# Kernel optimization log

Hardware: AMD Instinct MI355X
Metric: run time of the kernel (lower is better)

## Reference

```python
import jax, jax.numpy as jnp
import numpy as np

WS = 8          # window_size
NH = 8          # num_heads
DIM = 512
INNER = 512
CDIM = 128
CINNER = 128
SHIFTED = True
EPS = 1e-6
N = WS * WS     # tokens per window
SCALE = 1.0 / np.sqrt(INNER // NH + CINNER // NH)  # SDPA scale over fused (feat+coord) head dim


def _rmsnorm(x, g):
    return x * jax.lax.rsqrt(jnp.mean(x * x, axis=-1, keepdims=True) + EPS) * g


def _rel_indices():
    idx = np.array([[x, y] for x in range(WS) for y in range(WS)])
    ri = idx[None, :, :] - idx[:, None, :] + WS - 1
    return ri[..., 0], ri[..., 1]


def _shift_mask(Wh, Ww):
    s = WS
    k = s * (s // 2)
    row = np.zeros((N, N), np.float32)
    row[-k:, :-k] = -np.inf
    row[:-k, -k:] = -np.inf
    col = row.reshape(s, s, s, s).transpose(1, 0, 3, 2).reshape(N, N)
    m = np.zeros((Wh, Ww, N, N), np.float32)
    m[:, -1] += row
    m[-1, :] += col
    return jnp.asarray(m)


def setup_inputs() -> dict:
    key = jax.random.key(0)
    ks = jax.random.split(key, 16)
    B, h, w = 4, 128, 128

    def lin(k, fan_in, fan_out):
        return jax.random.normal(k, (fan_in, fan_out), jnp.float32) * (fan_in ** -0.5)

    return {
        "features": jax.random.normal(ks[0], (B, h, w, DIM), jnp.float32),
        "coords": jax.random.normal(ks[1], (B, h, w, CDIM), jnp.float32),
        "w_fqk": lin(ks[2], DIM, 2 * INNER),
        "b_fqk": jnp.zeros((2 * INNER,), jnp.float32),
        "g_fqk": jnp.ones((2 * INNER,), jnp.float32),
        "w_cqk": lin(ks[3], CDIM, 2 * CINNER),
        "b_cqk": jnp.zeros((2 * CINNER,), jnp.float32),
        "g_cqk": jnp.ones((2 * CINNER,), jnp.float32),
        "w_v": lin(ks[4], DIM, INNER),
        "b_v": jnp.zeros((INNER,), jnp.float32),
        "w_out": lin(ks[5], INNER, DIM),
        "b_out": jnp.zeros((DIM,), jnp.float32),
        "pos_emb": jax.random.normal(ks[6], (2 * WS - 1, 2 * WS - 1), jnp.float32),
    }


def reference(features, coords, w_fqk, b_fqk, g_fqk, w_cqk, b_cqk, g_cqk,
              w_v, b_v, w_out, b_out, pos_emb):
    B, h, w, _ = features.shape
    pad_h = (WS - h % WS) % WS
    pad_w = (WS - w % WS) % WS
    H_pad, W_pad = h + pad_h, w + pad_w
    Wh, Ww = H_pad // WS, W_pad // WS

    fqk = _rmsnorm(features @ w_fqk + b_fqk, g_fqk)
    f_q, f_k = jnp.split(fqk, 2, axis=-1)
    cqk = _rmsnorm(coords @ w_cqk + b_cqk, g_cqk)
    c_q, c_k = jnp.split(cqk, 2, axis=-1)
    f_v = features @ w_v + b_v

    def win(t):
        t = jnp.pad(t, ((0, 0), (0, pad_h), (0, pad_w), (0, 0)))
        if SHIFTED:
            t = jnp.roll(t, (-(WS // 2), -(WS // 2)), axis=(1, 2))
        D = t.shape[-1]
        t = t.reshape(B, Wh, WS, Ww, WS, D).transpose(0, 1, 3, 2, 4, 5)
        return t.reshape(B, Wh, Ww, N, D)

    def heads(t):
        D = t.shape[-1]
        return t.reshape(B, Wh, Ww, N, NH, D // NH)

    fq, fk, fv = heads(win(f_q)), heads(win(f_k)), heads(win(f_v))
    cq, ck = heads(win(c_q)), heads(win(c_k))

    # fused feature + coordinate QK scores, per head per window
    scores = (jnp.einsum('bxyqhd,bxykhd->bxyhqk', fq, fk)
              + jnp.einsum('bxyqhd,bxykhd->bxyhqk', cq, ck)) * SCALE

    ri0, ri1 = _rel_indices()
    pos_bias = pos_emb[ri0, ri1]  # (N, N)
    bias = pos_bias[None, None, None, None]
    if SHIFTED:
        bias = bias + _shift_mask(Wh, Ww)[None, :, :, None]
    scores = scores + bias

    attn = jax.nn.softmax(scores, axis=-1)
    out = jnp.einsum('bxyhqk,bxykhd->bxyqhd', attn, fv)
    out = out.reshape(B, Wh, Ww, N, INNER)

    # un-window
    out = out.reshape(B, Wh, Ww, WS, WS, INNER).transpose(0, 1, 3, 2, 4, 5)
    out = out.reshape(B, H_pad, W_pad, INNER)
    if SHIFTED:
        out = jnp.roll(out, (WS // 2, WS // 2), axis=(1, 2))
    out = out[:, :h, :w, :]
    return out @ w_out + b_out
```

## Files before the change

kernel.cpp:

```cpp
#include <hip/hip_runtime.h>
#include <hip/hip_bf16.h>
#include <type_traits>

using bf16 = __hip_bfloat16;
typedef __bf16 bf16x8 __attribute__((ext_vector_type(8)));
typedef float f32x4 __attribute__((ext_vector_type(4)));

static constexpr int TOKENS = 4 * 128 * 128;
#define SCALE_F 0.11180339887498949f
#define EPS_F 1e-6f

__device__ __forceinline__ float u2f(unsigned short u) {
  union { unsigned int i; float f; } c; c.i = (unsigned int)u << 16; return c.f;
}
__device__ __forceinline__ unsigned short f2u(float f) {
  bf16 h = __float2bfloat16(f); return *reinterpret_cast<unsigned short*>(&h);
}
__device__ __forceinline__ float b2f(bf16 v) { return __bfloat162float(v); }
__device__ __forceinline__ int4 cvt8(const float* p) {
  float4 a = ((const float4*)p)[0], b = ((const float4*)p)[1];
  union { int4 i4; unsigned short s[8]; } u;
  u.s[0] = f2u(a.x); u.s[1] = f2u(a.y); u.s[2] = f2u(a.z); u.s[3] = f2u(a.w);
  u.s[4] = f2u(b.x); u.s[5] = f2u(b.y); u.s[6] = f2u(b.z); u.s[7] = f2u(b.w);
  return u.i4;
}
__device__ __forceinline__ void gload16(const bf16* g, bf16* l) {
  __builtin_amdgcn_global_load_lds(
      (const __attribute__((address_space(1))) unsigned int*)g,
      (__attribute__((address_space(3))) unsigned int*)l, 16, 0, 0);
}

__global__ void convert_k(const float* __restrict__ in, bf16* __restrict__ out,
                          long n) {
  long i = ((long)blockIdx.x * 256 + threadIdx.x) * 8;
  long stride = (long)gridDim.x * 256 * 8;
  for (; i < n; i += stride) *(int4*)(out + i) = cvt8(in + i);
}

__global__ void transpose_k(const float* __restrict__ in, bf16* __restrict__ out,
                            int K, int N) {
  int i = blockIdx.x * 256 + threadIdx.x;
  if (i >= K * N) return;
  int k = i / N, n = i - k * N;
  out[(size_t)n * K + k] = __float2bfloat16(in[i]);
}

__global__ void biascat_k(const float* __restrict__ a, const float* __restrict__ b,
                          float* __restrict__ o) {
  int i = blockIdx.x * 256 + threadIdx.x;
  if (i < 1536) o[i] = i < 1024 ? a[i] : b[i - 1024];
}

__global__ void gains_k(const float* __restrict__ g_fqk,
                        const float* __restrict__ g_cqk,
                        float* __restrict__ gf, float* __restrict__ gc) {
  int i = blockIdx.x * 256 + threadIdx.x;
  if (i < 512) gf[i] = g_fqk[i] * g_fqk[512 + i];
  else if (i < 640) { int d = i - 512; gc[d] = g_cqk[d] * g_cqk[128 + d]; }
}

template <typename TC, int SSNX, int GS>
__global__ __launch_bounds__(512, 2) void gemm256p_k(
    const bf16* __restrict__ A, const bf16* __restrict__ Wt,
    const float* __restrict__ bias, TC* __restrict__ C,
    float* __restrict__ ssq, const float* __restrict__ gsc,
    int M, int N, int K) {
  extern __shared__ __align__(16) bf16 smem[];
  bf16* sW = smem;
  bf16* sX = smem + 32768;
  const int t = threadIdx.x, lane = t & 63, wave = t >> 6;
  const int wm = wave >> 2, wn = wave & 3;
  const int l15 = lane & 15, kg = lane >> 4;
  const int nwg = gridDim.x * gridDim.y;
  int id = blockIdx.y * gridDim.x + blockIdx.x;
  id = (id & 7) * (nwg >> 3) + (id >> 3);
  const int bx = id % gridDim.x, by = id / gridDim.x;
  const int bm = by * 256, bn = bx * 256;
  f32x4 acc[8][4] = {};

  const int lr = t >> 3, ch = t & 7;
  const int ssw = ((ch ^ (lr & 7)) * 8);
  const int rsw = (l15 & 7) * 8;

  auto stW = [&](int buf, int fh, int k0) {
#pragma unroll
    for (int g = 0; g < 2; ++g)
      gload16(Wt + (size_t)(bn + g * 128 + fh * 64 + lr) * K + k0 + ssw,
              sW + buf * 16384 + (fh * 128 + g * 64) * 64 + t * 8);
  };
  auto stX = [&](int buf, int th, int k0) {
#pragma unroll
    for (int g = 0; g < 2; ++g)
      gload16(A + (size_t)(bm + (g * 2 + (lr >> 5)) * 64 + th * 32 + (lr & 31)) * K + k0 + ssw,
              sX + buf * 16384 + (th * 128 + g * 64) * 64 + t * 8);
  };
  auto rdW = [&](int buf, int fh, int i, int ks) {
    int row = fh * 128 + wm * 64 + i * 16 + l15;
    return *(const bf16x8*)(sW + buf * 16384 + row * 64 + ((ks * 32 + kg * 8) ^ rsw));
  };
  auto rdX = [&](int buf, int th, int j, int ks) {
    int row = th * 128 + wn * 32 + j * 16 + l15;
    return *(const bf16x8*)(sX + buf * 16384 + row * 64 + ((ks * 32 + kg * 8) ^ rsw));
  };

  const int NT = K >> 6;
  stW(0, 0, 0); stX(0, 0, 0); stX(0, 1, 0); stW(0, 1, 0);

  bf16x8 wfr[4][2], xf0[2][2], xf1[2][2];
  for (int u = 0; u < NT; ++u) {
    const int buf = u & 1, nbuf = buf ^ 1, k1 = (u + 1) << 6;
    const bool pf = (u + 1 < NT);
    asm volatile("s_waitcnt vmcnt(4)" ::: "memory");
    __builtin_amdgcn_s_barrier();
    __builtin_amdgcn_sched_barrier(0);
#pragma unroll
    for (int i = 0; i < 4; ++i)
#pragma unroll
      for (int ks = 0; ks < 2; ++ks) wfr[i][ks] = rdW(buf, 0, i, ks);
#pragma unroll
    for (int j = 0; j < 2; ++j)
#pragma unroll
      for (int ks = 0; ks < 2; ++ks) xf0[j][ks] = rdX(buf, 0, j, ks);
    if (pf) { stW(nbuf, 0, k1); stX(nbuf, 0, k1); }
    asm volatile("s_waitcnt lgkmcnt(0)" ::: "memory");
    __builtin_amdgcn_sched_barrier(0);
    __builtin_amdgcn_s_setprio(1);
#pragma unroll
    for (int i = 0; i < 4; ++i)
#pragma unroll
      for (int j = 0; j < 2; ++j)
#pragma unroll
        for (int ks = 0; ks < 2; ++ks)
          acc[i][j] = __builtin_amdgcn_mfma_f32_16x16x32_bf16(wfr[i][ks], xf0[j][ks], acc[i][j], 0, 0, 0);
    __builtin_amdgcn_s_setprio(0);
    if (pf) asm volatile("s_waitcnt vmcnt(6)" ::: "memory");
    else    asm volatile("s_waitcnt vmcnt(2)" ::: "memory");
    __builtin_amdgcn_s_barrier();
    __builtin_amdgcn_sched_barrier(0);
#pragma unroll
    for (int j = 0; j < 2; ++j)
#pragma unroll
      for (int ks = 0; ks < 2; ++ks) xf1[j][ks] = rdX(buf, 1, j, ks);
    if (pf) stX(nbuf, 1, k1);
    asm volatile("s_waitcnt lgkmcnt(0)" ::: "memory");
    __builtin_amdgcn_sched_barrier(0);
    __builtin_amdgcn_s_setprio(1);
#pragma unroll
    for (int i = 0; i < 4; ++i)
#pragma unroll
      for (int j = 0; j < 2; ++j)
#pragma unroll
        for (int ks = 0; ks < 2; ++ks)
          acc[i][2 + j] = __builtin_amdgcn_mfma_f32_16x16x32_bf16(wfr[i][ks], xf1[j][ks], acc[i][2 + j], 0, 0, 0);
    __builtin_amdgcn_s_setprio(0);
    if (pf) asm volatile("s_waitcnt vmcnt(6)" ::: "memory");
    else    asm volatile("s_waitcnt vmcnt(0)" ::: "memory");
    __builtin_amdgcn_s_barrier();
    __builtin_amdgcn_sched_barrier(0);
#pragma unroll
    for (int i = 0; i < 4; ++i)
#pragma unroll
      for (int ks = 0; ks < 2; ++ks) wfr[i][ks] = rdW(buf, 1, i, ks);
    if (pf) stW(nbuf, 1, k1);
    asm volatile("s_waitcnt lgkmcnt(0)" ::: "memory");
    __builtin_amdgcn_sched_barrier(0);
    __builtin_amdgcn_s_setprio(1);
#pragma unroll
    for (int i = 0; i < 4; ++i)
#pragma unroll
      for (int j = 0; j < 2; ++j)
#pragma unroll
        for (int ks = 0; ks < 2; ++ks)
          acc[4 + i][j] = __builtin_amdgcn_mfma_f32_16x16x32_bf16(wfr[i][ks], xf0[j][ks], acc[4 + i][j], 0, 0, 0);
    __builtin_amdgcn_s_setprio(0);
    __builtin_amdgcn_s_barrier();
    __builtin_amdgcn_sched_barrier(0);
    __builtin_amdgcn_s_setprio(1);
#pragma unroll
    for (int i = 0; i < 4; ++i)
#pragma unroll
      for (int j = 0; j < 2; ++j)
#pragma unroll
        for (int ks = 0; ks < 2; ++ks)
          acc[4 + i][2 + j] = __builtin_amdgcn_mfma_f32_16x16x32_bf16(wfr[i][ks], xf1[j][ks], acc[4 + i][2 + j], 0, 0, 0);
    __builtin_amdgcn_s_setprio(0);
  }

  float bvi[8][4];
#pragma unroll
  for (int fi = 0; fi < 8; ++fi) {
    float4 b4 = *(const float4*)(bias + bn + wm * 128 + (fi >> 2) * 64 + (fi & 3) * 16 + kg * 4);
    bvi[fi][0] = b4.x; bvi[fi][1] = b4.y; bvi[fi][2] = b4.z; bvi[fi][3] = b4.w;
  }
#pragma unroll
  for (int tj = 0; tj < 4; ++tj) {
    const int token = bm + wn * 64 + (tj >> 1) * 32 + (tj & 1) * 16 + l15;
    float ssum = 0.f;
#pragma unroll
    for (int fi = 0; fi < 8; ++fi) {
      const int fo = wm * 128 + (fi >> 2) * 64 + (fi & 3) * 16 + kg * 4;
      float v0 = acc[fi][tj][0] + bvi[fi][0];
      float v1 = acc[fi][tj][1] + bvi[fi][1];
      float v2 = acc[fi][tj][2] + bvi[fi][2];
      float v3 = acc[fi][tj][3] + bvi[fi][3];
      if constexpr (SSNX > 0)
        ssum += v0 * v0 + v1 * v1 + v2 * v2 + v3 * v3;
      if constexpr (GS) {
        const int col = bn + fo;
        if (col >= 512 && col < 1024) {
          float4 g4 = *(const float4*)(gsc + (col - 512));
          v0 *= g4.x; v1 *= g4.y; v2 *= g4.z; v3 *= g4.w;
        }
      }
      const size_t off = (size_t)token * N + bn + fo;
      if constexpr (std::is_same<TC, float>::value) {
        *(float4*)(C + off) = float4{v0, v1, v2, v3};
      } else {
        ushort4 pk{f2u(v0), f2u(v1), f2u(v2), f2u(v3)};
        *(ushort4*)(C + off) = pk;
      }
    }
    if constexpr (SSNX > 0) {
      ssum += __shfl_xor(ssum, 16);
      ssum += __shfl_xor(ssum, 32);
      if (bx < SSNX && kg == 0)
        ssq[(size_t)token * (SSNX * 2) + bx * 2 + wm] = ssum;
    }
  }
}

template <typename TC, int SSNX, int GS>
__global__ __launch_bounds__(256) void gemm128_k(
    const bf16* __restrict__ A, const bf16* __restrict__ Wt,
    const float* __restrict__ bias, TC* __restrict__ C,
    float* __restrict__ ssq, const float* __restrict__ gsc,
    int M, int N, int K) {
  __shared__ __align__(16) bf16 sA[2][4096];
  __shared__ __align__(16) bf16 sB[2][4096];
  const int t = threadIdx.x, lane = t & 63, wave = t >> 6;
  const int wr = wave >> 1, wc = wave & 1;
  const int nwg = gridDim.x * gridDim.y;
  int id = blockIdx.y * gridDim.x + blockIdx.x;
  if ((nwg & 7) == 0) id = (id & 7) * (nwg >> 3) + (id >> 3);
  const int bx = id % gridDim.x, by = id / gridDim.x;
  const int bm = by * 128, bn = bx * 128;
  const int l15 = lane & 15, kg = lane >> 4;
  f32x4 acc[4][4] = {};

  const int srow = t >> 2;
  const int ske = ((t & 3) ^ ((srow >> 1) & 3)) * 8;
  const bf16* pA0 = A + (size_t)(bm + srow) * K + ske;
  const bf16* pA1 = A + (size_t)(bm + 64 + srow) * K + ske;
  const bf16* pB0 = Wt + (size_t)(bn + srow) * K + ske;
  const bf16* pB1 = Wt + (size_t)(bn + 64 + srow) * K + ske;
  const int wo = wave * 512;

  gload16(pA0, &sA[0][wo]);
  gload16(pA1, &sA[0][2048 + wo]);
  gload16(pB0, &sB[0][wo]);
  gload16(pB1, &sB[0][2048 + wo]);
  __syncthreads();

  const int nt = K >> 5;
  int cur = 0;
  for (int tt = 0; tt < nt; ++tt) {
    if (tt + 1 < nt) {
      pA0 += 32; pA1 += 32; pB0 += 32; pB1 += 32;
      gload16(pA0, &sA[cur ^ 1][wo]);
      gload16(pA1, &sA[cur ^ 1][2048 + wo]);
      gload16(pB0, &sB[cur ^ 1][wo]);
      gload16(pB1, &sB[cur ^ 1][2048 + wo]);
    }
    bf16x8 wf[4], xf[4];
#pragma unroll
    for (int i = 0; i < 4; ++i) {
      int frow = wc * 64 + i * 16 + l15;
      int xrow = wr * 64 + i * 16 + l15;
      wf[i] = *(const bf16x8*)(&sB[cur][frow * 32 + ((kg ^ ((frow >> 1) & 3)) * 8)]);
      xf[i] = *(const bf16x8*)(&sA[cur][xrow * 32 + ((kg ^ ((xrow >> 1) & 3)) * 8)]);
    }
#pragma unroll
    for (int i = 0; i < 4; ++i)
#pragma unroll
      for (int j = 0; j < 4; ++j)
        acc[i][j] = __builtin_amdgcn_mfma_f32_16x16x32_bf16(wf[i], xf[j], acc[i][j], 0, 0, 0);
    __syncthreads();
    cur ^= 1;
  }

  float bvi[4][4];
#pragma unroll
  for (int i = 0; i < 4; ++i) {
    float4 b4 = *(const float4*)(bias + bn + wc * 64 + i * 16 + kg * 4);
    bvi[i][0] = b4.x; bvi[i][1] = b4.y; bvi[i][2] = b4.z; bvi[i][3] = b4.w;
  }
#pragma unroll
  for (int j = 0; j < 4; ++j) {
    const int token = bm + wr * 64 + j * 16 + l15;
    float ssum = 0.f;
#pragma unroll
    for (int i = 0; i < 4; ++i) {
      const int fo = wc * 64 + i * 16 + kg * 4;
      float v0 = acc[i][j][0] + bvi[i][0];
      float v1 = acc[i][j][1] + bvi[i][1];
      float v2 = acc[i][j][2] + bvi[i][2];
      float v3 = acc[i][j][3] + bvi[i][3];
      if constexpr (SSNX > 0)
        ssum += v0 * v0 + v1 * v1 + v2 * v2 + v3 * v3;
      if constexpr (GS) {
        const int col = bn + fo;
        if (col >= 128 && col < 256) {
          float4 g4 = *(const float4*)(gsc + (col - 128));
          v0 *= g4.x; v1 *= g4.y; v2 *= g4.z; v3 *= g4.w;
        }
      }
      const size_t off = (size_t)token * N + bn + fo;
      if constexpr (std::is_same<TC, float>::value) {
        *(float4*)(C + off) = float4{v0, v1, v2, v3};
      } else {
        ushort4 pk{f2u(v0), f2u(v1), f2u(v2), f2u(v3)};
        *(ushort4*)(C + off) = pk;
      }
    }
    if constexpr (SSNX > 0) {
      ssum += __shfl_xor(ssum, 16);
      ssum += __shfl_xor(ssum, 32);
      if (bx < SSNX && kg == 0)
        ssq[(size_t)token * (SSNX * 2) + bx * 2 + wc] = ssum;
    }
  }
}

__global__ void finalize_rs_k(const float* __restrict__ pf,
                              const float* __restrict__ pc,
                              float* __restrict__ rsf, float* __restrict__ rsc) {
  int i = blockIdx.x * 256 + threadIdx.x;
  if (i >= TOKENS) return;
  float s = 0.f;
#pragma unroll
  for (int j = 0; j < 8; ++j) s += pf[(size_t)i * 8 + j];
  rsf[i] = rsqrtf(s * (1.f / 1024.f) + EPS_F);
  float c = 0.f;
#pragma unroll
  for (int j = 0; j < 4; ++j) c += pc[(size_t)i * 4 + j];
  rsc[i] = rsqrtf(c * (1.f / 256.f) + EPS_F);
}

__global__ __launch_bounds__(256) void attn_mfma_k(
    const bf16* __restrict__ qkv, const bf16* __restrict__ cqk,
    const float* __restrict__ pos, const float* __restrict__ rs_f,
    const float* __restrict__ rs_c, bf16* __restrict__ aout) {
  __shared__ __align__(16) bf16 sQ[64][104], sK[64][104];
  __shared__ __align__(16) bf16 sVt[64][72];
  __shared__ __align__(16) bf16 sP[64][72];
  __shared__ float sPos[15][15];
  __shared__ float sRsF[64], sRsC[64];
  const int t = threadIdx.x, lane = t & 63, wave = t >> 6;
  const int head = blockIdx.x & 7;
  const int wid = blockIdx.x >> 3;
  const int wx = wid & 15, wy = (wid >> 4) & 15, b = wid >> 8;

  for (int i = t; i < 225; i += 256) sPos[i / 15][i % 15] = pos[i];
  if (t < 64) {
    const int y = ((wy << 3) + (t >> 3) + 4) & 127;
    const int x = ((wx << 3) + (t & 7) + 4) & 127;
    const size_t tok = ((size_t)b << 14) | (y << 7) | x;
    sRsF[t] = rs_f[tok];
    sRsC[t] = rs_c[tok];
  }
  {
    const int n = t >> 2, p = t & 3;
    const int y = ((wy << 3) + (n >> 3) + 4) & 127;
    const int x = ((wx << 3) + (n & 7) + 4) & 127;
    const size_t tok = ((size_t)b << 14) | (y << 7) | x;
    const bf16* row = qkv + tok * 1536;
    const int4* qp = (const int4*)(row + head * 64 + p * 16);
    ((int4*)&sQ[n][p * 16])[0] = qp[0];
    ((int4*)&sQ[n][p * 16])[1] = qp[1];
    const int4* kp = (const int4*)(row + 512 + head * 64 + p * 16);
    ((int4*)&sK[n][p * 16])[0] = kp[0];
    ((int4*)&sK[n][p * 16])[1] = kp[1];
    const bf16* vp = row + 1024 + head * 64 + p * 16;
#pragma unroll
    for (int i = 0; i < 16; ++i) sVt[p * 16 + i][n] = vp[i];
    const bf16* crow = cqk + tok * 256;
    if (p == 0) {
      const int4* cp = (const int4*)(crow + head * 16);
      ((int4*)&sQ[n][64])[0] = cp[0];
      ((int4*)&sQ[n][64])[1] = cp[1];
    } else if (p == 1) {
      const int4* cp = (const int4*)(crow + 128 + head * 16);
      ((int4*)&sK[n][64])[0] = cp[0];
      ((int4*)&sK[n][64])[1] = cp[1];
    } else if (p == 2) {
      ((int4*)&sQ[n][80])[0] = int4{0, 0, 0, 0};
      ((int4*)&sQ[n][80])[1] = int4{0, 0, 0, 0};
    } else {
      ((int4*)&sK[n][80])[0] = int4{0, 0, 0, 0};
      ((int4*)&sK[n][80])[1] = int4{0, 0, 0, 0};
    }
  }
  __syncthreads();

  const int l15 = lane & 15, kg = lane >> 4;
  bf16x8 qa[3];
#pragma unroll
  for (int ko = 0; ko < 3; ++ko)
    qa[ko] = *(const bf16x8*)&sQ[wave * 16 + l15][ko * 32 + kg * 8];
  f32x4 saccf[4] = {}, saccc[4] = {};
#pragma unroll
  for (int j = 0; j < 4; ++j) {
#pragma unroll
    for (int ko = 0; ko < 2; ++ko) {
      bf16x8 kb = *(const bf16x8*)&sK[j * 16 + l15][ko * 32 + kg * 8];
      saccf[j] = __builtin_amdgcn_mfma_f32_16x16x32_bf16(qa[ko], kb, saccf[j], 0, 0, 0);
    }
    bf16x8 kb2 = *(const bf16x8*)&sK[j * 16 + l15][64 + kg * 8];
    saccc[j] = __builtin_amdgcn_mfma_f32_16x16x32_bf16(qa[2], kb2, saccc[j], 0, 0, 0);
  }

  const bool lastx = (wx == 15), lasty = (wy == 15);
  float rqf[4], rqc[4];
#pragma unroll
  for (int r = 0; r < 4; ++r) {
    rqf[r] = sRsF[wave * 16 + kg * 4 + r];
    rqc[r] = sRsC[wave * 16 + kg * 4 + r];
  }
  float sv[4][4], mx[4], sum[4], inv[4];
#pragma unroll
  for (int r = 0; r < 4; ++r) mx[r] = -1e30f;
#pragma unroll
  for (int j = 0; j < 4; ++j) {
    int kcol = j * 16 + l15, kh = kcol >> 3, kw = kcol & 7;
    float rkf = sRsF[kcol], rkc = sRsC[kcol];
#pragma unroll
    for (int r = 0; r < 4; ++r) {
      int q = wave * 16 + kg * 4 + r, qh = q >> 3, qw = q & 7;
      bool msk = (lastx && ((qh >= 4) != (kh >= 4))) ||
                 (lasty && ((qw >= 4) != (kw >= 4)));
      float raw = saccf[j][r] * rqf[r] * rkf + saccc[j][r] * rqc[r] * rkc;
      float val = msk ? -1e30f : raw * SCALE_F + sPos[kh - qh + 7][kw - qw + 7];
      sv[j][r] = val;
      mx[r] = fmaxf(mx[r], val);
    }
  }
#pragma unroll
  for (int m = 1; m < 16; m <<= 1)
#pragma unroll
    for (int r = 0; r < 4; ++r) mx[r] = fmaxf(mx[r], __shfl_xor(mx[r], m));
#pragma unroll
  for (int r = 0; r < 4; ++r) sum[r] = 0.f;
#pragma unroll
  for (int j = 0; j < 4; ++j) {
    int kcol = j * 16 + l15;
#pragma unroll
    for (int r = 0; r < 4; ++r) {
      float e = __expf(sv[j][r] - mx[r]);
      sum[r] += e;
      sP[wave * 16 + kg * 4 + r][kcol] = __float2bfloat16(e);
    }
  }
#pragma unroll
  for (int m = 1; m < 16; m <<= 1)
#pragma unroll
    for (int r = 0; r < 4; ++r) sum[r] += __shfl_xor(sum[r], m);
#pragma unroll
  for (int r = 0; r < 4; ++r) inv[r] = 1.f / sum[r];
  __syncthreads();

  bf16x8 pa[2];
#pragma unroll
  for (int ko = 0; ko < 2; ++ko)
    pa[ko] = *(const bf16x8*)&sP[wave * 16 + l15][ko * 32 + kg * 8];
  f32x4 oacc[4] = {};
#pragma unroll
  for (int jf = 0; jf < 4; ++jf)
#pragma unroll
    for (int ko = 0; ko < 2; ++ko) {
      bf16x8 vb = *(const bf16x8*)&sVt[jf * 16 + l15][ko * 32 + kg * 8];
      oacc[jf] = __builtin_amdgcn_mfma_f32_16x16x32_bf16(pa[ko], vb, oacc[jf], 0, 0, 0);
    }
#pragma unroll
  for (int r = 0; r < 4; ++r) {
    int q = wave * 16 + kg * 4 + r;
    const int y = ((wy << 3) + (q >> 3) + 4) & 127;
    const int x = ((wx << 3) + (q & 7) + 4) & 127;
    const size_t tok = ((size_t)b << 14) | (y << 7) | x;
    bf16* dst = aout + tok * 512 + head * 64;
#pragma unroll
    for (int jf = 0; jf < 4; ++jf)
      dst[jf * 16 + l15] = __float2bfloat16(oacc[jf][r] * inv[r]);
  }
}

extern "C" void kernel_launch(void* const* d_in, const int* in_sizes, int n_in,
                              void* d_out, int out_size, void* d_ws, size_t ws_size,
                              hipStream_t stream) {
  const float* features = (const float*)d_in[0];
  const float* coords   = (const float*)d_in[1];
  const float* w_fqk = (const float*)d_in[2];
  const float* b_fqk = (const float*)d_in[3];
  const float* g_fqk = (const float*)d_in[4];
  const float* w_cqk = (const float*)d_in[5];
  const float* b_cqk = (const float*)d_in[6];
  const float* g_cqk = (const float*)d_in[7];
  const float* w_v   = (const float*)d_in[8];
  const float* b_v   = (const float*)d_in[9];
  const float* w_out = (const float*)d_in[10];
  const float* b_out = (const float*)d_in[11];
  const float* pos_emb = (const float*)d_in[12];
  float* out = (float*)d_out;

  const int M = TOKENS;
  bf16* qkv   = (bf16*)d_ws;
  bf16* cqk   = qkv + (size_t)M * 1536;
  bf16* aout  = cqk + (size_t)M * 256;
  bf16* wcombT = aout + (size_t)M * 512;
  bf16* wcqkT  = wcombT + (size_t)1536 * 512;
  bf16* woutT  = wcqkT + 256 * 128;
  float* bias_comb = (float*)(woutT + 512 * 512);
  float* ssq_f = bias_comb + 1536;
  float* ssq_c = ssq_f + (size_t)M * 8;
  float* rs_f  = ssq_c + (size_t)M * 4;
  float* rs_c  = rs_f + M;
  float* gf    = rs_c + M;
  float* gc    = gf + 512;
  bf16* fb16 = (bf16*)d_out;
  bf16* cb16 = fb16 + (size_t)M * 512;

  convert_k<<<2048, 256, 0, stream>>>(features, fb16, (long)M * 512);
  convert_k<<<1024, 256, 0, stream>>>(coords, cb16, (long)M * 128);
  transpose_k<<<(512 * 1024 + 255) / 256, 256, 0, stream>>>(w_fqk, wcombT, 512, 1024);
  transpose_k<<<(512 * 512 + 255) / 256, 256, 0, stream>>>(w_v, wcombT + (size_t)1024 * 512, 512, 512);
  transpose_k<<<(128 * 256 + 255) / 256, 256, 0, stream>>>(w_cqk, wcqkT, 128, 256);
  transpose_k<<<(512 * 512 + 255) / 256, 256, 0, stream>>>(w_out, woutT, 512, 512);
  biascat_k<<<6, 256, 0, stream>>>(b_fqk, b_v, bias_comb);
  gains_k<<<3, 256, 0, stream>>>(g_fqk, g_cqk, gf, gc);

  gemm256p_k<bf16, 4, 1><<<dim3(6, 256), 512, 131072, stream>>>(fb16, wcombT, bias_comb, qkv, ssq_f, gf, M, 1536, 512);
  gemm128_k<bf16, 2, 1><<<dim3(2, 512), 256, 0, stream>>>(cb16, wcqkT, b_cqk, cqk, ssq_c, gc, M, 256, 128);
  finalize_rs_k<<<TOKENS / 256, 256, 0, stream>>>(ssq_f, ssq_c, rs_f, rs_c);
  attn_mfma_k<<<4 * 16 * 16 * 8, 256, 0, stream>>>(qkv, cqk, pos_emb, rs_f, rs_c, aout);
  gemm256p_k<float, 0, 0><<<dim3(2, 256), 512, 131072, stream>>>(aout, woutT, b_out, out, nullptr, nullptr, M, 512, 512);
}
```

Baseline: 380.7 us.

## Make GEMM persistent across N tiles with a triple-buffered K=32 pipeline

Replaces the 2D-grid 256x256 GEMM with a kernel where each block owns 256 rows and loops over every N tile (6 for the QKV projection, 2 for the output projection). It uses a 3-stage ring of K=32 slices so global loads run two steps ahead and the pipeline does not drain between N tiles. Bias is staged in LDS once per block. This reduces the grid to 256 blocks with a smaller LDS footprint. The intent is to hide the per-tile prologue/epilogue and keep A rows hot. In exchange there is less parallelism (256 blocks, one wave of work per CU) and a serialized epilogue between tiles. The ssq stride changes to 12, but finalize still reads only 8 of the entries.

```diff
diff --git a/kernel.cpp b/kernel.cpp
--- a/kernel.cpp
+++ b/kernel.cpp
@@ -59,172 +59,138 @@
   else if (i < 640) { int d = i - 512; gc[d] = g_cqk[d] * g_cqk[128 + d]; }
 }
 
-template <typename TC, int SSNX, int GS>
-__global__ __launch_bounds__(512, 2) void gemm256p_k(
+template <typename TC, int EPSSQ, int TPB, int GS>
+__global__ __launch_bounds__(512) void gemm256s_k(
     const bf16* __restrict__ A, const bf16* __restrict__ Wt,
     const float* __restrict__ bias, TC* __restrict__ C,
-    float* __restrict__ ssq, const float* __restrict__ gsc,
-    int M, int N, int K) {
+    float* __restrict__ ssq, const float* __restrict__ gsc, int N) {
+  constexpr int K = 512, GT = 16 * TPB;
   extern __shared__ __align__(16) bf16 smem[];
-  bf16* sW = smem;
-  bf16* sX = smem + 32768;
+  bf16* sX = smem;
+  bf16* sW = smem + 24576;
+  float* sB = (float*)(smem + 49152);
   const int t = threadIdx.x, lane = t & 63, wave = t >> 6;
   const int wm = wave >> 2, wn = wave & 3;
   const int l15 = lane & 15, kg = lane >> 4;
-  const int nwg = gridDim.x * gridDim.y;
-  int id = blockIdx.y * gridDim.x + blockIdx.x;
-  id = (id & 7) * (nwg >> 3) + (id >> 3);
-  const int bx = id % gridDim.x, by = id / gridDim.x;
-  const int bm = by * 256, bn = bx * 256;
+  const int bm = blockIdx.x * 256;
+  const int srow = t >> 2;
+  const int ssw = ((t & 3) ^ ((srow >> 1) & 3)) * 8;
+  const int sdst = t * 8;
+
+  auto stX = [&](int buf, int g) {
+    int k0 = (g & 15) << 5;
+    bf16* d = sX + buf * 8192 + sdst;
+    gload16(A + (size_t)(bm + srow) * K + k0 + ssw, d);
+    gload16(A + (size_t)(bm + 128 + srow) * K + k0 + ssw, d + 4096);
+  };
+  auto stW = [&](int buf, int g) {
+    int k0 = (g & 15) << 5;
+    int bn = (g >> 4) << 8;
+    bf16* d = sW + buf * 8192 + sdst;
+    gload16(Wt + (size_t)(bn + srow) * K + k0 + ssw, d);
+    gload16(Wt + (size_t)(bn + 128 + srow) * K + k0 + ssw, d + 4096);
+  };
+  auto rdX = [&](int buf, int j) {
+    int row = wn * 64 + j * 16 + l15;
+    return *(const bf16x8*)(sX + buf * 8192 + row * 32 + ((kg ^ ((row >> 1) & 3)) * 8));
+  };
+  auto rdW = [&](int buf, int half, int i) {
+    int row = wm * 128 + half * 64 + i * 16 + l15;
+    return *(const bf16x8*)(sW + buf * 8192 + row * 32 + ((kg ^ ((row >> 1) & 3)) * 8));
+  };
+
+  const int nb4 = N / 4;
+  float4 bv4 = float4{0.f, 0.f, 0.f, 0.f};
+  if (t < nb4) bv4 = ((const float4*)bias)[t];
+  stX(0, 0); stW(0, 0); stX(1, 1); stW(1, 1);
+  asm volatile("s_waitcnt vmcnt(8)" ::: "memory");
+  if (t < nb4) ((float4*)sB)[t] = bv4;
+
   f32x4 acc[8][4] = {};
-
-  const int lr = t >> 3, ch = t & 7;
-  const int ssw = ((ch ^ (lr & 7)) * 8);
-  const int rsw = (l15 & 7) * 8;
-
-  auto stW = [&](int buf, int fh, int k0) {
-#pragma unroll
-    for (int g = 0; g < 2; ++g)
-      gload16(Wt + (size_t)(bn + g * 128 + fh * 64 + lr) * K + k0 + ssw,
-              sW + buf * 16384 + (fh * 128 + g * 64) * 64 + t * 8);
-  };
-  auto stX = [&](int buf, int th, int k0) {
-#pragma unroll
-    for (int g = 0; g < 2; ++g)
-      gload16(A + (size_t)(bm + (g * 2 + (lr >> 5)) * 64 + th * 32 + (lr & 31)) * K + k0 + ssw,
-              sX + buf * 16384 + (th * 128 + g * 64) * 64 + t * 8);
-  };
-  auto rdW = [&](int buf, int fh, int i, int ks) {
-    int row = fh * 128 + wm * 64 + i * 16 + l15;
-    return *(const bf16x8*)(sW + buf * 16384 + row * 64 + ((ks * 32 + kg * 8) ^ rsw));
-  };
-  auto rdX = [&](int buf, int th, int j, int ks) {
-    int row = th * 128 + wn * 32 + j * 16 + l15;
-    return *(const bf16x8*)(sX + buf * 16384 + row * 64 + ((ks * 32 + kg * 8) ^ rsw));
-  };
-
-  const int NT = K >> 6;
-  stW(0, 0, 0); stX(0, 0, 0); stX(0, 1, 0); stW(0, 1, 0);
-
-  bf16x8 wfr[4][2], xf0[2][2], xf1[2][2];
-  for (int u = 0; u < NT; ++u) {
-    const int buf = u & 1, nbuf = buf ^ 1, k1 = (u + 1) << 6;
-    const bool pf = (u + 1 < NT);
-    asm volatile("s_waitcnt vmcnt(4)" ::: "memory");
+  int buf = 0;
+  for (int g = 0; g < GT; ++g) {
+    if (g == GT - 1 || (g > 0 && (g & 15) == 0)) {
+      asm volatile("s_waitcnt vmcnt(0)" ::: "memory");
+    } else {
+      asm volatile("s_waitcnt vmcnt(4)" ::: "memory");
+    }
     __builtin_amdgcn_s_barrier();
     __builtin_amdgcn_sched_barrier(0);
-#pragma unroll
-    for (int i = 0; i < 4; ++i)
-#pragma unroll
-      for (int ks = 0; ks < 2; ++ks) wfr[i][ks] = rdW(buf, 0, i, ks);
-#pragma unroll
-    for (int j = 0; j < 2; ++j)
-#pragma unroll
-      for (int ks = 0; ks < 2; ++ks) xf0[j][ks] = rdX(buf, 0, j, ks);
-    if (pf) { stW(nbuf, 0, k1); stX(nbuf, 0, k1); }
+    int nb = buf + 2; if (nb >= 3) nb -= 3;
+    bf16x8 xf[4], wf[4];
+#pragma unroll
+    for (int j = 0; j < 4; ++j) xf[j] = rdX(buf, j);
+#pragma unroll
+    for (int i = 0; i < 4; ++i) wf[i] = rdW(buf, 0, i);
+    if (g + 2 < GT) stX(nb, g + 2);
     asm volatile("s_waitcnt lgkmcnt(0)" ::: "memory");
     __builtin_amdgcn_sched_barrier(0);
     __builtin_amdgcn_s_setprio(1);
 #pragma unroll
     for (int i = 0; i < 4; ++i)
 #pragma unroll
-      for (int j = 0; j < 2; ++j)
-#pragma unroll
-        for (int ks = 0; ks < 2; ++ks)
-          acc[i][j] = __builtin_amdgcn_mfma_f32_16x16x32_bf16(wfr[i][ks], xf0[j][ks], acc[i][j], 0, 0, 0);
+      for (int j = 0; j < 4; ++j)
+        acc[i][j] = __builtin_amdgcn_mfma_f32_16x16x32_bf16(wf[i], xf[j], acc[i][j], 0, 0, 0);
     __builtin_amdgcn_s_setprio(0);
-    if (pf) asm volatile("s_waitcnt vmcnt(6)" ::: "memory");
-    else    asm volatile("s_waitcnt vmcnt(2)" ::: "memory");
     __builtin_amdgcn_s_barrier();
     __builtin_amdgcn_sched_barrier(0);
 #pragma unroll
-    for (int j = 0; j < 2; ++j)
-#pragma unroll
-      for (int ks = 0; ks < 2; ++ks) xf1[j][ks] = rdX(buf, 1, j, ks);
-    if (pf) stX(nbuf, 1, k1);
+    for (int i = 0; i < 4; ++i) wf[i] = rdW(buf, 1, i);
+    if (g + 2 < GT) stW(nb, g + 2);
     asm volatile("s_waitcnt lgkmcnt(0)" ::: "memory");
     __builtin_amdgcn_sched_barrier(0);
     __builtin_amdgcn_s_setprio(1);
 #pragma unroll
     for (int i = 0; i < 4; ++i)
 #pragma unroll
-      for (int j = 0; j < 2; ++j)
-#pragma unroll
-        for (int ks = 0; ks < 2; ++ks)
-          acc[i][2 + j] = __builtin_amdgcn_mfma_f32_16x16x32_bf16(wfr[i][ks], xf1[j][ks], acc[i][2 + j], 0, 0, 0);
+      for (int j = 0; j < 4; ++j)
+        acc[4 + i][j] = __builtin_amdgcn_mfma_f32_16x16x32_bf16(wf[i], xf[j], acc[4 + i][j], 0, 0, 0);
     __builtin_amdgcn_s_setprio(0);
-    if (pf) asm volatile("s_waitcnt vmcnt(6)" ::: "memory");
-    else    asm volatile("s_waitcnt vmcnt(0)" ::: "memory");
-    __builtin_amdgcn_s_barrier();
-    __builtin_amdgcn_sched_barrier(0);
-#pragma unroll
-    for (int i = 0; i < 4; ++i)
-#pragma unroll
-      for (int ks = 0; ks < 2; ++ks) wfr[i][ks] = rdW(buf, 1, i, ks);
-    if (pf) stW(nbuf, 1, k1);
-    asm volatile("s_waitcnt lgkmcnt(0)" ::: "memory");
-    __builtin_amdgcn_sched_barrier(0);
-    __builtin_amdgcn_s_setprio(1);
-#pragma unroll
-    for (int i = 0; i < 4; ++i)
-#pragma unroll
-      for (int j = 0; j < 2; ++j)
-#pragma unroll
-        for (int ks = 0; ks < 2; ++ks)
-          acc[4 + i][j] = __builtin_amdgcn_mfma_f32_16x16x32_bf16(wfr[i][ks], xf0[j][ks], acc[4 + i][j], 0, 0, 0);
-    __builtin_amdgcn_s_setprio(0);
-    __builtin_amdgcn_s_barrier();
-    __builtin_amdgcn_sched_barrier(0);
-    __builtin_amdgcn_s_setprio(1);
-#pragma unroll
-    for (int i = 0; i < 4; ++i)
-#pragma unroll
-      for (int j = 0; j < 2; ++j)
-#pragma unroll
-        for (int ks = 0; ks < 2; ++ks)
-          acc[4 + i][2 + j] = __builtin_amdgcn_mfma_f32_16x16x32_bf16(wfr[i][ks], xf1[j][ks], acc[4 + i][2 + j], 0, 0, 0);
-    __builtin_amdgcn_s_setprio(0);
-  }
-
-  float bvi[8][4];
-#pragma unroll
-  for (int fi = 0; fi < 8; ++fi) {
-    float4 b4 = *(const float4*)(bias + bn + wm * 128 + (fi >> 2) * 64 + (fi & 3) * 16 + kg * 4);
-    bvi[fi][0] = b4.x; bvi[fi][1] = b4.y; bvi[fi][2] = b4.z; bvi[fi][3] = b4.w;
-  }
-#pragma unroll
-  for (int tj = 0; tj < 4; ++tj) {
-    const int token = bm + wn * 64 + (tj >> 1) * 32 + (tj & 1) * 16 + l15;
-    float ssum = 0.f;
-#pragma unroll
-    for (int fi = 0; fi < 8; ++fi) {
-      const int fo = wm * 128 + (fi >> 2) * 64 + (fi & 3) * 16 + kg * 4;
-      float v0 = acc[fi][tj][0] + bvi[fi][0];
-      float v1 = acc[fi][tj][1] + bvi[fi][1];
-      float v2 = acc[fi][tj][2] + bvi[fi][2];
-      float v3 = acc[fi][tj][3] + bvi[fi][3];
-      if constexpr (SSNX > 0)
-        ssum += v0 * v0 + v1 * v1 + v2 * v2 + v3 * v3;
-      if constexpr (GS) {
-        const int col = bn + fo;
-        if (col >= 512 && col < 1024) {
-          float4 g4 = *(const float4*)(gsc + (col - 512));
-          v0 *= g4.x; v1 *= g4.y; v2 *= g4.z; v3 *= g4.w;
+    buf = buf + 1; if (buf >= 3) buf = 0;
+
+    if ((g & 15) == 15) {
+      const int tile = g >> 4;
+      const int bn = tile << 8;
+#pragma unroll
+      for (int tj = 0; tj < 4; ++tj) {
+        const int token = bm + wn * 64 + tj * 16 + l15;
+        float ssum = 0.f;
+#pragma unroll
+        for (int fi = 0; fi < 8; ++fi) {
+          const int fo = wm * 128 + (fi >> 2) * 64 + (fi & 3) * 16 + kg * 4;
+          float4 b4 = *(const float4*)(sB + bn + fo);
+          float v0 = acc[fi][tj][0] + b4.x;
+          float v1 = acc[fi][tj][1] + b4.y;
+          float v2 = acc[fi][tj][2] + b4.z;
+          float v3 = acc[fi][tj][3] + b4.w;
+          if constexpr (EPSSQ)
+            ssum += v0 * v0 + v1 * v1 + v2 * v2 + v3 * v3;
+          if constexpr (GS) {
+            const int col = bn + fo;
+            if (col >= 512 && col < 1024) {
+              float4 g4 = *(const float4*)(gsc + (col - 512));
+              v0 *= g4.x; v1 *= g4.y; v2 *= g4.z; v3 *= g4.w;
+            }
+          }
+          const size_t off = (size_t)token * N + bn + fo;
+          if constexpr (std::is_same<TC, float>::value) {
+            *(float4*)(C + off) = float4{v0, v1, v2, v3};
+          } else {
+            ushort4 pk{f2u(v0), f2u(v1), f2u(v2), f2u(v3)};
+            *(ushort4*)(C + off) = pk;
+          }
+        }
+        if constexpr (EPSSQ) {
+          ssum += __shfl_xor(ssum, 16);
+          ssum += __shfl_xor(ssum, 32);
+          if (kg == 0)
+            ssq[(size_t)token * (TPB * 2) + tile * 2 + wm] = ssum;
         }
       }
-      const size_t off = (size_t)token * N + bn + fo;
-      if constexpr (std::is_same<TC, float>::value) {
-        *(float4*)(C + off) = float4{v0, v1, v2, v3};
-      } else {
-        ushort4 pk{f2u(v0), f2u(v1), f2u(v2), f2u(v3)};
-        *(ushort4*)(C + off) = pk;
-      }
-    }
-    if constexpr (SSNX > 0) {
-      ssum += __shfl_xor(ssum, 16);
-      ssum += __shfl_xor(ssum, 32);
-      if (bx < SSNX && kg == 0)
-        ssq[(size_t)token * (SSNX * 2) + bx * 2 + wm] = ssum;
+#pragma unroll
+      for (int fi = 0; fi < 8; ++fi)
+#pragma unroll
+        for (int tj = 0; tj < 4; ++tj) acc[fi][tj] = f32x4{0.f, 0.f, 0.f, 0.f};
     }
   }
 }
@@ -338,7 +304,7 @@
   if (i >= TOKENS) return;
   float s = 0.f;
 #pragma unroll
-  for (int j = 0; j < 8; ++j) s += pf[(size_t)i * 8 + j];
+  for (int j = 0; j < 8; ++j) s += pf[(size_t)i * 12 + j];
   rsf[i] = rsqrtf(s * (1.f / 1024.f) + EPS_F);
   float c = 0.f;
 #pragma unroll
@@ -520,7 +486,7 @@
   bf16* woutT  = wcqkT + 256 * 128;
   float* bias_comb = (float*)(woutT + 512 * 512);
   float* ssq_f = bias_comb + 1536;
-  float* ssq_c = ssq_f + (size_t)M * 8;
+  float* ssq_c = ssq_f + (size_t)M * 12;
   float* rs_f  = ssq_c + (size_t)M * 4;
   float* rs_c  = rs_f + M;
   float* gf    = rs_c + M;
@@ -537,9 +503,9 @@
   biascat_k<<<6, 256, 0, stream>>>(b_fqk, b_v, bias_comb);
   gains_k<<<3, 256, 0, stream>>>(g_fqk, g_cqk, gf, gc);
 
-  gemm256p_k<bf16, 4, 1><<<dim3(6, 256), 512, 131072, stream>>>(fb16, wcombT, bias_comb, qkv, ssq_f, gf, M, 1536, 512);
+  gemm256s_k<bf16, 1, 6, 1><<<256, 512, 104448, stream>>>(fb16, wcombT, bias_comb, qkv, ssq_f, gf, 1536);
   gemm128_k<bf16, 2, 1><<<dim3(2, 512), 256, 0, stream>>>(cb16, wcqkT, b_cqk, cqk, ssq_c, gc, M, 256, 128);
   finalize_rs_k<<<TOKENS / 256, 256, 0, stream>>>(ssq_f, ssq_c, rs_f, rs_c);
   attn_mfma_k<<<4 * 16 * 16 * 8, 256, 0, stream>>>(qkv, cqk, pos_emb, rs_f, rs_c, aout);
-  gemm256p_k<float, 0, 0><<<dim3(2, 256), 512, 131072, stream>>>(aout, woutT, b_out, out, nullptr, nullptr, M, 512, 512);
-}
+  gemm256s_k<float, 0, 2, 0><<<256, 512, 100352, stream>>>(aout, woutT, b_out, out, nullptr, nullptr, 512);
+}
```

New measurement: 396.3 us. +4.1%, slower.
